# Optimization experiments

Measured on AMD Instinct MI355X. Metric: run time of the kernel, lower is better.

Reference implementation:

```python
import jax, jax.numpy as jnp
import numpy as np

T, B, V, H = 128, 64, 8192, 2048

def setup_inputs() -> dict:
    key = jax.random.key(0)
    k1, k2, k3, k4, k5 = jax.random.split(key, 5)
    inputs = jax.random.randint(k1, (T, B), 0, V, dtype=jnp.int64)
    hidden_w = jax.random.normal(k2, (H, V + H), dtype=jnp.float32) * 0.02
    hidden_b = jax.random.normal(k3, (H,), dtype=jnp.float32) * 0.02
    output_w = jax.random.normal(k4, (V, H), dtype=jnp.float32) * 0.02
    output_b = jax.random.normal(k5, (V,), dtype=jnp.float32) * 0.02
    return {"inputs": inputs, "hidden_w": hidden_w, "hidden_b": hidden_b,
            "output_w": output_w, "output_b": output_b}

def reference(inputs, hidden_w, hidden_b, output_w, output_b):
    vocab = output_w.shape[0]
    num_hiddens = hidden_w.shape[0]
    batch = inputs.shape[1]
    state0 = jnp.zeros((batch, num_hiddens), dtype=jnp.float32)

    def step(state, x):
        # x: (B,) int token ids -> one-hot (B, V)
        emb = jax.nn.one_hot(x, vocab, dtype=jnp.float32)
        combined = jnp.concatenate([emb, state], axis=1)       # (B, V+H)
        new_state = jnp.tanh(combined @ hidden_w.T + hidden_b)  # (B, H)
        out = new_state @ output_w.T + output_b                 # (B, V)
        return new_state, out

    final_state, outputs = jax.lax.scan(step, state0, inputs)
    # outputs: (T, B, V) — stacked version of the original's list of per-step outputs
    return outputs, final_state
```

## Files before the change

kernel.cpp:

```cpp
#include <hip/hip_runtime.h>

#define T_STEPS 128
#define BATCH   64
#define VOCAB   8192
#define HID     2048
#define WROW    (VOCAB + HID)
#define BH      (BATCH * HID)
#define CNT_STRIDE 512

typedef __bf16 bf16_t;
typedef __bf16 bf16x8 __attribute__((ext_vector_type(8)));
typedef float  f32x4  __attribute__((ext_vector_type(4)));
typedef unsigned long long u64;
typedef const __attribute__((address_space(1))) unsigned int gu32;
typedef __attribute__((address_space(3))) unsigned int lu32;

__global__ void conv_whh(const float* __restrict__ hw, bf16_t* __restrict__ whh,
                         int* __restrict__ cnt) {
    if (blockIdx.x == 0) {
        for (int i = threadIdx.x; i < 4 * CNT_STRIDE; i += 256) cnt[i] = 0;
    }
    int idx = blockIdx.x * 256 + threadIdx.x;
    int i4 = idx * 4;
    int h = i4 >> 11;
    int j = i4 & 2047;
    float4 w = *(const float4*)(hw + (size_t)h * WROW + VOCAB + j);
    union { bf16_t b[4]; uint2 u; } t;
    t.b[0] = (bf16_t)w.x; t.b[1] = (bf16_t)w.y; t.b[2] = (bf16_t)w.z; t.b[3] = (bf16_t)w.w;
    *(uint2*)(whh + (size_t)h * HID + j) = t.u;
}

__global__ void conv_wout(const float* __restrict__ wo, bf16_t* __restrict__ wob) {
    size_t i4 = ((size_t)blockIdx.x * 256 + threadIdx.x) * 4;
    float4 w = *(const float4*)(wo + i4);
    union { bf16_t b[4]; uint2 u; } t;
    t.b[0] = (bf16_t)w.x; t.b[1] = (bf16_t)w.y; t.b[2] = (bf16_t)w.z; t.b[3] = (bf16_t)w.w;
    *(uint2*)(wob + i4) = t.u;
}

__global__ void trans_emb(const float* __restrict__ hw, bf16_t* __restrict__ wt) {
    __shared__ float tile[32][33];
    int tx = threadIdx.x, ty = threadIdx.y;
    int v0 = blockIdx.x * 32, h0 = blockIdx.y * 32;
#pragma unroll
    for (int i = 0; i < 4; i++)
        tile[ty + i * 8][tx] = hw[(size_t)(h0 + ty + i * 8) * WROW + v0 + tx];
    __syncthreads();
#pragma unroll
    for (int i = 0; i < 4; i++)
        wt[(size_t)(v0 + ty + i * 8) * HID + h0 + tx] = (bf16_t)tile[tx][ty + i * 8];
}

__launch_bounds__(512)
__global__ void rnn_persist(bf16_t* __restrict__ states,
                            const bf16_t* __restrict__ whh,
                            const bf16_t* __restrict__ wembT,
                            const float* __restrict__ hb,
                            const int* __restrict__ toks,
                            float* __restrict__ fin,
                            int* __restrict__ cnt) {
    __shared__ float part[8][512];

    const int tid = threadIdx.x;
    const int w = tid >> 6, lane = tid & 63;
    const int q = lane >> 4, l15 = lane & 15;
    const int bm = blockIdx.x & 3, bn = blockIdx.x >> 2;
    const int m0 = bm * 16, n0 = bn * 32;
    const int kb = w * 256;

    bf16x8 breg[2][8];
#pragma unroll
    for (int nt = 0; nt < 2; nt++)
#pragma unroll
        for (int kk = 0; kk < 8; kk++)
            breg[nt][kk] = *(const bf16x8*)(
                whh + (size_t)(n0 + nt * 16 + l15) * HID + kb + kk * 32 + q * 8);

    const size_t abase8 = (size_t)((m0 + l15) * HID + kb + q * 8) >> 2;

    const int er = tid >> 4, ec = (tid & 15) * 2;
    const int R = m0 + er, h = n0 + ec;
    float bias0 = 0.f, bias1 = 0.f;
    if (tid < 256) { bias0 = hb[h]; bias1 = hb[h + 1]; }
    int* flags = cnt + bm * 64;

    for (int t = 0; t < T_STEPS; ++t) {
        float emb0 = 0.f, emb1 = 0.f;
        if (tid < 256) {
            int tok = toks[t * BATCH + R];
            union { unsigned int u; bf16_t b[2]; } e;
            e.u = *(const unsigned int*)(wembT + (size_t)tok * HID + h);
            emb0 = (float)e.b[0]; emb1 = (float)e.b[1];
        }

        f32x4 acc0 = (f32x4){0.f, 0.f, 0.f, 0.f};
        f32x4 acc1 = (f32x4){0.f, 0.f, 0.f, 0.f};
        if (t > 0) {
            if (w == 0) {
                int v;
                do {
                    v = __hip_atomic_load(&flags[lane], __ATOMIC_RELAXED,
                                          __HIP_MEMORY_SCOPE_SYSTEM);
                } while (!__all(v >= t));
            }
            __syncthreads();
            asm volatile("" ::: "memory");

            const u64* sprev = (const u64*)(states + (size_t)t * BH);
            u64 a8[16];
#pragma unroll
            for (int kk = 0; kk < 8; kk++) {
                a8[2 * kk]     = __hip_atomic_load(sprev + abase8 + kk * 8,
                                    __ATOMIC_RELAXED, __HIP_MEMORY_SCOPE_SYSTEM);
                a8[2 * kk + 1] = __hip_atomic_load(sprev + abase8 + kk * 8 + 1,
                                    __ATOMIC_RELAXED, __HIP_MEMORY_SCOPE_SYSTEM);
            }
#pragma unroll
            for (int kk = 0; kk < 8; kk++) {
                union { u64 u[2]; bf16x8 v; } cv;
                cv.u[0] = a8[2 * kk]; cv.u[1] = a8[2 * kk + 1];
                acc0 = __builtin_amdgcn_mfma_f32_16x16x32_bf16(cv.v, breg[0][kk], acc0, 0, 0, 0);
                acc1 = __builtin_amdgcn_mfma_f32_16x16x32_bf16(cv.v, breg[1][kk], acc1, 0, 0, 0);
            }
        }
#pragma unroll
        for (int i = 0; i < 4; i++) {
            part[w][(q * 4 + i) * 32 + l15]      = acc0[i];
            part[w][(q * 4 + i) * 32 + 16 + l15] = acc1[i];
        }
        __syncthreads();
        if (tid < 256) {
            float s0 = 0.f, s1 = 0.f;
#pragma unroll
            for (int ww = 0; ww < 8; ww++) {
                float2 p = *(const float2*)&part[ww][er * 32 + ec];
                s0 += p.x; s1 += p.y;
            }
            float v0 = tanhf(s0 + emb0 + bias0);
            float v1 = tanhf(s1 + emb1 + bias1);
            union { bf16_t b[2]; unsigned int u; } pk;
            pk.b[0] = (bf16_t)v0; pk.b[1] = (bf16_t)v1;
            __hip_atomic_store(
                (unsigned int*)(states + (size_t)(t + 1) * BH + R * HID + h),
                pk.u, __ATOMIC_RELAXED, __HIP_MEMORY_SCOPE_SYSTEM);
            if (t == T_STEPS - 1)
                *(float2*)&fin[R * HID + h] = make_float2(v0, v1);
        }
        __syncthreads();
        asm volatile("" ::: "memory");
        if (tid == 0)
            __hip_atomic_store(&flags[bn], t + 1, __ATOMIC_RELAXED,
                               __HIP_MEMORY_SCOPE_SYSTEM);
    }
}

__launch_bounds__(256)
__global__ void out_gemm(const bf16_t* __restrict__ A,
                         const bf16_t* __restrict__ Bw,
                         const float* __restrict__ bias,
                         float* __restrict__ out) {
    __shared__ bf16_t As[2][128 * 32];
    __shared__ bf16_t Bs[2][128 * 32];
    const int tid = threadIdx.x;
    const int wv = tid >> 6, lane = tid & 63;
    const int wm = wv >> 1, wn = wv & 1;
    const int q = lane >> 4, l15 = lane & 15;
    const int bm = blockIdx.y, bn = blockIdx.x;

    const bf16_t* gA = A  + (size_t)bm * 128 * 2048;
    const bf16_t* gB = Bw + (size_t)bn * 128 * 2048;

    const int sRow = lane >> 2;
    const int sCol = (lane & 3) * 8;

#define STAGE_TILE(dstBuf, gsrc, k0)                                          \
    do {                                                                      \
        _Pragma("unroll")                                                     \
        for (int i_ = 0; i_ < 2; i_++) {                                      \
            int chunk_ = i_ * 4 + wv;                                         \
            __builtin_amdgcn_global_load_lds(                                 \
                (gu32*)(gsrc + ((size_t)(chunk_ * 16 + sRow)) * 2048 + (k0) + sCol), \
                (lu32*)(dstBuf + chunk_ * 16 * 32), 16, 0, 0);                \
        }                                                                     \
    } while (0)

    f32x4 acc[4][4];
#pragma unroll
    for (int mt = 0; mt < 4; mt++)
#pragma unroll
        for (int nt = 0; nt < 4; nt++)
            acc[mt][nt] = (f32x4){0.f, 0.f, 0.f, 0.f};

    STAGE_TILE(As[0], gA, 0);
    STAGE_TILE(Bs[0], gB, 0);
    __syncthreads();

    for (int it = 0; it < 64; ++it) {
        int cur = it & 1;
        if (it < 63) {
            int k0 = (it + 1) * 32;
            STAGE_TILE(As[cur ^ 1], gA, k0);
            STAGE_TILE(Bs[cur ^ 1], gB, k0);
        }
        bf16x8 af[4], bfr[4];
#pragma unroll
        for (int mt = 0; mt < 4; mt++)
            af[mt] = *(const bf16x8*)&As[cur][(wm * 64 + mt * 16 + l15) * 32 + q * 8];
#pragma unroll
        for (int nt = 0; nt < 4; nt++)
            bfr[nt] = *(const bf16x8*)&Bs[cur][(wn * 64 + nt * 16 + l15) * 32 + q * 8];
#pragma unroll
        for (int mt = 0; mt < 4; mt++)
#pragma unroll
            for (int nt = 0; nt < 4; nt++)
                acc[mt][nt] = __builtin_amdgcn_mfma_f32_16x16x32_bf16(
                    af[mt], bfr[nt], acc[mt][nt], 0, 0, 0);
        __syncthreads();
    }
#undef STAGE_TILE

#pragma unroll
    for (int nt = 0; nt < 4; nt++) {
        int col = bn * 128 + wn * 64 + nt * 16 + l15;
        float bv = bias[col];
#pragma unroll
        for (int mt = 0; mt < 4; mt++) {
#pragma unroll
            for (int i = 0; i < 4; i++) {
                int row = bm * 128 + wm * 64 + mt * 16 + q * 4 + i;
                out[(size_t)row * 8192 + col] = acc[mt][nt][i] + bv;
            }
        }
    }
}

extern "C" void kernel_launch(void* const* d_in, const int* in_sizes, int n_in,
                              void* d_out, int out_size, void* d_ws, size_t ws_size,
                              hipStream_t stream) {
    const int*   toks = (const int*)d_in[0];
    const float* hw   = (const float*)d_in[1];
    const float* hb   = (const float*)d_in[2];
    const float* wo   = (const float*)d_in[3];
    const float* ob   = (const float*)d_in[4];
    float* out = (float*)d_out;

    char* ws = (char*)d_ws;
    bf16_t* states = (bf16_t*)ws;
    bf16_t* whh    = (bf16_t*)(ws + 33816576ULL);
    bf16_t* woutb  = (bf16_t*)(ws + 33816576ULL + 8388608ULL);
    bf16_t* wembT  = (bf16_t*)(ws + 33816576ULL + 8388608ULL + 33554432ULL);
    int*    cnt    = (int*)ws;

    conv_whh<<<(HID * HID / 4) / 256, 256, 0, stream>>>(hw, whh, cnt);
    conv_wout<<<(VOCAB * HID / 4) / 256, 256, 0, stream>>>(wo, woutb);
    trans_emb<<<dim3(VOCAB / 32, HID / 32), dim3(32, 8), 0, stream>>>(hw, wembT);

    float* fin = out + (size_t)T_STEPS * BATCH * VOCAB;
    void* args[] = { (void*)&states, (void*)&whh, (void*)&wembT,
                     (void*)&hb, (void*)&toks, (void*)&fin, (void*)&cnt };
    hipLaunchCooperativeKernel((void*)rnn_persist, dim3(256), dim3(512),
                               args, 0, stream);

    out_gemm<<<dim3(64, 64), 256, 0, stream>>>(
        states + (size_t)BH, woutb, ob, out);
}
```

Before: 1.359 ms.

## Fuse output projection GEMM into persistent RNN kernel to overlap with recurrence

Removes the separate output GEMM kernel and folds its 128x128 tiles into the persistent cooperative RNN kernel. Each block interleaves chunks of output tiles between recurrence steps once the needed state rows are published, then finishes the remaining tiles after the time loop. The aim is to hide the output projection behind the latency-bound sequential recurrence. In exchange the GEMM uses smaller per-block tiles, loads A through system-scope atomics, and adds extra barriers and flag polling inside the recurrence loop, which could lengthen the critical path.

```diff
diff --git a/kernel.cpp b/kernel.cpp
--- a/kernel.cpp
+++ b/kernel.cpp
@@ -14,6 +14,8 @@
 typedef unsigned long long u64;
 typedef const __attribute__((address_space(1))) unsigned int gu32;
 typedef __attribute__((address_space(3))) unsigned int lu32;
+
+#define LOAD_SYS(p) __hip_atomic_load((p), __ATOMIC_RELAXED, __HIP_MEMORY_SCOPE_SYSTEM)
 
 __global__ void conv_whh(const float* __restrict__ hw, bf16_t* __restrict__ whh,
                          int* __restrict__ cnt) {
@@ -52,14 +54,21 @@
 }
 
 __launch_bounds__(512)
-__global__ void rnn_persist(bf16_t* __restrict__ states,
-                            const bf16_t* __restrict__ whh,
-                            const bf16_t* __restrict__ wembT,
-                            const float* __restrict__ hb,
-                            const int* __restrict__ toks,
-                            float* __restrict__ fin,
-                            int* __restrict__ cnt) {
-    __shared__ float part[8][512];
+__global__ void rnn_fused(bf16_t* __restrict__ states,
+                          const bf16_t* __restrict__ whh,
+                          const bf16_t* __restrict__ wembT,
+                          const float* __restrict__ hb,
+                          const int* __restrict__ toks,
+                          float* __restrict__ fin,
+                          int* __restrict__ cnt,
+                          const bf16_t* __restrict__ woutb,
+                          const float* __restrict__ obias,
+                          float* __restrict__ out) {
+    __shared__ union {
+        float part[8][512];
+        struct { bf16_t A[2][4096]; bf16_t B[2][4096]; } g;
+    } sh;
+    __shared__ int s_ready;
 
     const int tid = threadIdx.x;
     const int w = tid >> 6, lane = tid & 63;
@@ -83,6 +92,81 @@
     float bias0 = 0.f, bias1 = 0.f;
     if (tid < 256) { bias0 = hb[h]; bias1 = hb[h + 1]; }
     int* flags = cnt + bm * 64;
+
+    const int wm = w >> 2, wn = w & 3;
+    const int sRow = tid >> 2, sCol = (tid & 3) * 8;
+    const u64* A64 = (const u64*)(states + (size_t)BH);
+    f32x4 gacc[4][2];
+    int gj = 0, gkq = 0, gact = 0, gbm = 0, gbn = 0;
+
+#define GEMM_CHUNK()                                                           \
+  do {                                                                         \
+    const size_t ab_ = (((size_t)(gbm * 128 + sRow)) << 9) + (size_t)((tid & 3) * 2); \
+    const bf16_t* gBp_ = woutb + (size_t)gbn * 128 * 2048;                     \
+    u64 s0_ = LOAD_SYS(A64 + ab_ + gkq * 8);                                   \
+    u64 s1_ = LOAD_SYS(A64 + ab_ + gkq * 8 + 1);                               \
+    __builtin_amdgcn_global_load_lds(                                          \
+        (gu32*)(gBp_ + (size_t)sRow * 2048 + gkq * 32 + sCol),                 \
+        (lu32*)&sh.g.B[0][w * 512], 16, 0, 0);                                 \
+    *(u64*)&sh.g.A[0][tid * 8]     = s0_;                                      \
+    *(u64*)&sh.g.A[0][tid * 8 + 4] = s1_;                                      \
+    __syncthreads();                                                           \
+    for (int it_ = 0; it_ < 8; ++it_) {                                        \
+      int cur_ = it_ & 1;                                                      \
+      u64 na0_ = 0, na1_ = 0;                                                  \
+      if (it_ < 7) {                                                           \
+        int kk_ = gkq + it_ + 1;                                               \
+        na0_ = LOAD_SYS(A64 + ab_ + kk_ * 8);                                  \
+        na1_ = LOAD_SYS(A64 + ab_ + kk_ * 8 + 1);                              \
+        __builtin_amdgcn_global_load_lds(                                      \
+            (gu32*)(gBp_ + (size_t)sRow * 2048 + kk_ * 32 + sCol),             \
+            (lu32*)&sh.g.B[cur_ ^ 1][w * 512], 16, 0, 0);                      \
+      }                                                                        \
+      bf16x8 af_[4], bf_[2];                                                   \
+      _Pragma("unroll")                                                        \
+      for (int mt_ = 0; mt_ < 4; mt_++)                                        \
+        af_[mt_] = *(const bf16x8*)&sh.g.A[cur_][(wm * 64 + mt_ * 16 + l15) * 32 + q * 8]; \
+      _Pragma("unroll")                                                        \
+      for (int nt_ = 0; nt_ < 2; nt_++)                                        \
+        bf_[nt_] = *(const bf16x8*)&sh.g.B[cur_][(wn * 32 + nt_ * 16 + l15) * 32 + q * 8]; \
+      _Pragma("unroll")                                                        \
+      for (int mt_ = 0; mt_ < 4; mt_++)                                        \
+        _Pragma("unroll")                                                      \
+        for (int nt_ = 0; nt_ < 2; nt_++)                                      \
+          gacc[mt_][nt_] = __builtin_amdgcn_mfma_f32_16x16x32_bf16(            \
+              af_[mt_], bf_[nt_], gacc[mt_][nt_], 0, 0, 0);                    \
+      if (it_ < 7) {                                                           \
+        *(u64*)&sh.g.A[cur_ ^ 1][tid * 8]     = na0_;                          \
+        *(u64*)&sh.g.A[cur_ ^ 1][tid * 8 + 4] = na1_;                          \
+      }                                                                        \
+      __syncthreads();                                                         \
+    }                                                                          \
+  } while (0)
+
+#define GEMM_WRITE_C()                                                         \
+  do {                                                                         \
+    _Pragma("unroll")                                                          \
+    for (int nt_ = 0; nt_ < 2; nt_++) {                                        \
+      int col_ = gbn * 128 + wn * 32 + nt_ * 16 + l15;                         \
+      float bv_ = obias[col_];                                                 \
+      _Pragma("unroll")                                                        \
+      for (int mt_ = 0; mt_ < 4; mt_++)                                        \
+        _Pragma("unroll")                                                      \
+        for (int i_ = 0; i_ < 4; i_++) {                                       \
+          int row_ = gbm * 128 + wm * 64 + mt_ * 16 + q * 4 + i_;              \
+          out[(size_t)row_ * 8192 + col_] = gacc[mt_][nt_][i_] + bv_;          \
+        }                                                                      \
+    }                                                                          \
+  } while (0)
+
+#define GEMM_ZERO_ACC()                                                        \
+  do {                                                                         \
+    _Pragma("unroll")                                                          \
+    for (int mt_ = 0; mt_ < 4; mt_++)                                          \
+      _Pragma("unroll")                                                        \
+      for (int nt_ = 0; nt_ < 2; nt_++)                                        \
+        gacc[mt_][nt_] = (f32x4){0.f, 0.f, 0.f, 0.f};                          \
+  } while (0)
 
     for (int t = 0; t < T_STEPS; ++t) {
         float emb0 = 0.f, emb1 = 0.f;
@@ -99,8 +183,7 @@
             if (w == 0) {
                 int v;
                 do {
-                    v = __hip_atomic_load(&flags[lane], __ATOMIC_RELAXED,
-                                          __HIP_MEMORY_SCOPE_SYSTEM);
+                    v = LOAD_SYS(&flags[lane]);
                 } while (!__all(v >= t));
             }
             __syncthreads();
@@ -110,10 +193,8 @@
             u64 a8[16];
 #pragma unroll
             for (int kk = 0; kk < 8; kk++) {
-                a8[2 * kk]     = __hip_atomic_load(sprev + abase8 + kk * 8,
-                                    __ATOMIC_RELAXED, __HIP_MEMORY_SCOPE_SYSTEM);
-                a8[2 * kk + 1] = __hip_atomic_load(sprev + abase8 + kk * 8 + 1,
-                                    __ATOMIC_RELAXED, __HIP_MEMORY_SCOPE_SYSTEM);
+                a8[2 * kk]     = LOAD_SYS(sprev + abase8 + kk * 8);
+                a8[2 * kk + 1] = LOAD_SYS(sprev + abase8 + kk * 8 + 1);
             }
 #pragma unroll
             for (int kk = 0; kk < 8; kk++) {
@@ -125,15 +206,15 @@
         }
 #pragma unroll
         for (int i = 0; i < 4; i++) {
-            part[w][(q * 4 + i) * 32 + l15]      = acc0[i];
-            part[w][(q * 4 + i) * 32 + 16 + l15] = acc1[i];
+            sh.part[w][(q * 4 + i) * 32 + l15]      = acc0[i];
+            sh.part[w][(q * 4 + i) * 32 + 16 + l15] = acc1[i];
         }
         __syncthreads();
         if (tid < 256) {
             float s0 = 0.f, s1 = 0.f;
 #pragma unroll
             for (int ww = 0; ww < 8; ww++) {
-                float2 p = *(const float2*)&part[ww][er * 32 + ec];
+                float2 p = *(const float2*)&sh.part[ww][er * 32 + ec];
                 s0 += p.x; s1 += p.y;
             }
             float v0 = tanhf(s0 + emb0 + bias0);
@@ -151,87 +232,67 @@
         if (tid == 0)
             __hip_atomic_store(&flags[bn], t + 1, __ATOMIC_RELAXED,
                                __HIP_MEMORY_SCOPE_SYSTEM);
+
+        if (gj < 16) {
+            int nch = (gj * 8 + (gkq >> 3) <= t) ? 2 : 1;
+            for (int c = 0; c < nch; ++c) {
+                if (!gact) {
+                    int tile = gj * 256 + blockIdx.x;
+                    gbm = tile >> 6; gbn = tile & 63;
+                    if (w == 0) {
+                        int f0 = LOAD_SYS(&cnt[lane]);
+                        int f1 = LOAD_SYS(&cnt[64 + lane]);
+                        int f2 = LOAD_SYS(&cnt[128 + lane]);
+                        int f3 = LOAD_SYS(&cnt[192 + lane]);
+                        int m01 = f0 < f1 ? f0 : f1;
+                        int m23 = f2 < f3 ? f2 : f3;
+                        int m = m01 < m23 ? m01 : m23;
+                        int r = __all(m >= 2 * gbm + 2) ? 1 : 0;
+                        if (lane == 0) s_ready = r;
+                    }
+                    __syncthreads();
+                    int ok = s_ready;
+                    __syncthreads();
+                    if (!ok) break;
+                    gact = 1; gkq = 0;
+                    GEMM_ZERO_ACC();
+                }
+                GEMM_CHUNK();
+                gkq += 8;
+                if (gkq == 64) { GEMM_WRITE_C(); gact = 0; gj++; break; }
+            }
+        }
     }
-}
-
-__launch_bounds__(256)
-__global__ void out_gemm(const bf16_t* __restrict__ A,
-                         const bf16_t* __restrict__ Bw,
-                         const float* __restrict__ bias,
-                         float* __restrict__ out) {
-    __shared__ bf16_t As[2][128 * 32];
-    __shared__ bf16_t Bs[2][128 * 32];
-    const int tid = threadIdx.x;
-    const int wv = tid >> 6, lane = tid & 63;
-    const int wm = wv >> 1, wn = wv & 1;
-    const int q = lane >> 4, l15 = lane & 15;
-    const int bm = blockIdx.y, bn = blockIdx.x;
-
-    const bf16_t* gA = A  + (size_t)bm * 128 * 2048;
-    const bf16_t* gB = Bw + (size_t)bn * 128 * 2048;
-
-    const int sRow = lane >> 2;
-    const int sCol = (lane & 3) * 8;
-
-#define STAGE_TILE(dstBuf, gsrc, k0)                                          \
-    do {                                                                      \
-        _Pragma("unroll")                                                     \
-        for (int i_ = 0; i_ < 2; i_++) {                                      \
-            int chunk_ = i_ * 4 + wv;                                         \
-            __builtin_amdgcn_global_load_lds(                                 \
-                (gu32*)(gsrc + ((size_t)(chunk_ * 16 + sRow)) * 2048 + (k0) + sCol), \
-                (lu32*)(dstBuf + chunk_ * 16 * 32), 16, 0, 0);                \
-        }                                                                     \
-    } while (0)
-
-    f32x4 acc[4][4];
-#pragma unroll
-    for (int mt = 0; mt < 4; mt++)
-#pragma unroll
-        for (int nt = 0; nt < 4; nt++)
-            acc[mt][nt] = (f32x4){0.f, 0.f, 0.f, 0.f};
-
-    STAGE_TILE(As[0], gA, 0);
-    STAGE_TILE(Bs[0], gB, 0);
-    __syncthreads();
-
-    for (int it = 0; it < 64; ++it) {
-        int cur = it & 1;
-        if (it < 63) {
-            int k0 = (it + 1) * 32;
-            STAGE_TILE(As[cur ^ 1], gA, k0);
-            STAGE_TILE(Bs[cur ^ 1], gB, k0);
-        }
-        bf16x8 af[4], bfr[4];
-#pragma unroll
-        for (int mt = 0; mt < 4; mt++)
-            af[mt] = *(const bf16x8*)&As[cur][(wm * 64 + mt * 16 + l15) * 32 + q * 8];
-#pragma unroll
-        for (int nt = 0; nt < 4; nt++)
-            bfr[nt] = *(const bf16x8*)&Bs[cur][(wn * 64 + nt * 16 + l15) * 32 + q * 8];
-#pragma unroll
-        for (int mt = 0; mt < 4; mt++)
-#pragma unroll
-            for (int nt = 0; nt < 4; nt++)
-                acc[mt][nt] = __builtin_amdgcn_mfma_f32_16x16x32_bf16(
-                    af[mt], bfr[nt], acc[mt][nt], 0, 0, 0);
-        __syncthreads();
+
+    while (gj < 16) {
+        if (!gact) {
+            int tile = gj * 256 + blockIdx.x;
+            gbm = tile >> 6; gbn = tile & 63;
+            if (w == 0) {
+                for (;;) {
+                    int f0 = LOAD_SYS(&cnt[lane]);
+                    int f1 = LOAD_SYS(&cnt[64 + lane]);
+                    int f2 = LOAD_SYS(&cnt[128 + lane]);
+                    int f3 = LOAD_SYS(&cnt[192 + lane]);
+                    int m01 = f0 < f1 ? f0 : f1;
+                    int m23 = f2 < f3 ? f2 : f3;
+                    int m = m01 < m23 ? m01 : m23;
+                    if (__all(m >= 2 * gbm + 2)) break;
+                    __builtin_amdgcn_s_sleep(8);
+                }
+            }
+            __syncthreads();
+            asm volatile("" ::: "memory");
+            gact = 1; gkq = 0;
+            GEMM_ZERO_ACC();
+        }
+        while (gkq < 64) { GEMM_CHUNK(); gkq += 8; }
+        GEMM_WRITE_C();
+        gact = 0; gj++;
     }
-#undef STAGE_TILE
-
-#pragma unroll
-    for (int nt = 0; nt < 4; nt++) {
-        int col = bn * 128 + wn * 64 + nt * 16 + l15;
-        float bv = bias[col];
-#pragma unroll
-        for (int mt = 0; mt < 4; mt++) {
-#pragma unroll
-            for (int i = 0; i < 4; i++) {
-                int row = bm * 128 + wm * 64 + mt * 16 + q * 4 + i;
-                out[(size_t)row * 8192 + col] = acc[mt][nt][i] + bv;
-            }
-        }
-    }
+#undef GEMM_CHUNK
+#undef GEMM_WRITE_C
+#undef GEMM_ZERO_ACC
 }
 
 extern "C" void kernel_launch(void* const* d_in, const int* in_sizes, int n_in,
@@ -257,10 +318,8 @@
 
     float* fin = out + (size_t)T_STEPS * BATCH * VOCAB;
     void* args[] = { (void*)&states, (void*)&whh, (void*)&wembT,
-                     (void*)&hb, (void*)&toks, (void*)&fin, (void*)&cnt };
-    hipLaunchCooperativeKernel((void*)rnn_persist, dim3(256), dim3(512),
+                     (void*)&hb, (void*)&toks, (void*)&fin, (void*)&cnt,
+                     (void*)&woutb, (void*)&ob, (void*)&out };
+    hipLaunchCooperativeKernel((void*)rnn_fused, dim3(256), dim3(512),
                                args, 0, stream);
-
-    out_gemm<<<dim3(64, 64), 256, 0, stream>>>(
-        states + (size_t)BH, woutb, ob, out);
-}
+}
```

After: 3.885 ms. 186% more time.
